# Kernel tuning notes

Hardware: AMD Instinct MI355X
Metric: run time of the kernel (lower is better)

Reference implementation:

```python
import jax, jax.numpy as jnp
import numpy as np

DIM = 1024
INNER = DIM // 2
DSTATE = 8
KSZ = 3
DTRANK = max(INNER // 8, 4)
B, L = 4, 4096


def setup_inputs() -> dict:
    key = jax.random.key(0)
    ks = jax.random.split(key, 8)
    s = 0.02
    x = jax.random.normal(ks[0], (B, L, DIM), dtype=jnp.float32)
    W_in = jax.random.normal(ks[1], (DIM, DIM), dtype=jnp.float32) * s
    Kx = jax.random.normal(ks[2], (INNER, 1, KSZ), dtype=jnp.float32) * 0.1
    Kz = jax.random.normal(ks[3], (INNER, 1, KSZ), dtype=jnp.float32) * 0.1
    W_xproj = jax.random.normal(ks[4], (DTRANK + 2 * DSTATE, INNER), dtype=jnp.float32) * s
    W_dt = jax.random.normal(ks[5], (INNER, DTRANK), dtype=jnp.float32) * s
    # dt bias: inverse_softplus of exp(linspace(log dt_min, log dt_max))
    dt_init = jnp.exp(jnp.linspace(jnp.log(0.02), jnp.log(0.2), INNER))
    b_dt = jnp.log(jnp.expm1(dt_init)).astype(jnp.float32)
    A_log = jnp.log(jnp.tile(jnp.arange(1, DSTATE + 1, dtype=jnp.float32), (INNER, 1)))
    D = jnp.ones((INNER,), dtype=jnp.float32)
    W_out = jax.random.normal(ks[6], (DIM, DIM), dtype=jnp.float32) * s
    return {"x": x, "W_in": W_in, "Kx": Kx, "Kz": Kz, "W_xproj": W_xproj,
            "W_dt": W_dt, "b_dt": b_dt, "A_log": A_log, "D": D, "W_out": W_out}


def _dwconv_silu(u, kern):
    # u: [B,L,C], kern: [C,1,K] depthwise (groups=C), 'same' padding
    c = u.shape[-1]
    v = jnp.transpose(u, (0, 2, 1))  # [B,C,L]
    v = jax.lax.conv_general_dilated(v, kern, (1,), [(KSZ // 2, KSZ // 2)],
                                     dimension_numbers=("NCH", "OIH", "NCH"),
                                     feature_group_count=c)
    return jax.nn.silu(jnp.transpose(v, (0, 2, 1)))


def _forward(x, W_in, Kx, Kz, W_xproj, W_dt, b_dt, A_log, D, W_out):
    h = jnp.einsum("bld,ed->ble", x, W_in)  # Linear(dim,dim), no bias
    xb, zb = jnp.split(h, 2, axis=-1)       # [B,L,INNER] each
    xb = _dwconv_silu(xb, Kx)
    zb = _dwconv_silu(zb, Kz)
    proj = jnp.einsum("blc,oc->blo", xb, W_xproj)
    dt_raw = proj[..., :DTRANK]
    b_raw = proj[..., DTRANK:DTRANK + DSTATE]
    c_raw = proj[..., DTRANK + DSTATE:]
    delta = jnp.clip(jax.nn.softplus(jnp.einsum("blr,cr->blc", dt_raw, W_dt) + b_dt), 1e-4, 1.0)  # [B,L,C]
    b_term = jnp.tanh(b_raw)  # [B,L,N]
    c_term = jnp.tanh(c_raw)  # [B,L,N]
    a = jax.nn.softplus(A_log) + 1e-4  # [C,N]
    decay = jnp.clip(jnp.exp(-delta[..., None] * a), 1e-4, 1.0)        # [B,L,C,N]
    drive = (1.0 - decay) * (b_term[:, :, None, :] * xb[..., None])    # [B,L,C,N]

    def step(state, inp):
        dec_t, drv_t, c_t, x_t = inp  # [B,C,N], [B,C,N], [B,N], [B,C]
        state = dec_t * state + drv_t
        y = jnp.sum(state * c_t[:, None, :], axis=-1) + D * x_t  # [B,C]
        return state, y

    tm = lambda t: jnp.moveaxis(t, 1, 0)  # time-major
    state0 = jnp.zeros((x.shape[0], INNER, DSTATE), dtype=jnp.float32)
    _, ys = jax.lax.scan(step, state0, (tm(decay), tm(drive), tm(c_term), tm(xb)))
    y = jnp.moveaxis(ys, 0, 1)  # [B,L,INNER]
    return jnp.einsum("bld,ed->ble", jnp.concatenate([y, zb], axis=-1), W_out)


def reference(x, W_in, Kx, Kz, W_xproj, W_dt, b_dt, A_log, D, W_out):
    return _forward(x, W_in, Kx, Kz, W_xproj, W_dt, b_dt, A_log, D, W_out)
```

## Files before the change

kernel.cpp:

```cpp
#include <hip/hip_runtime.h>


using bf16x8 = __attribute__((ext_vector_type(8))) short;
using f32x4  = __attribute__((ext_vector_type(4))) float;

__device__ __forceinline__ unsigned short f2bf(float f) {
  unsigned int u = __float_as_uint(f);
  u = u + 0x7fffu + ((u >> 16) & 1u);
  return (unsigned short)(u >> 16);
}

__device__ __forceinline__ float fsoftplus(float x) {
  return (x > 15.f) ? x : __logf(1.f + __expf(x));
}

__device__ __forceinline__ float ftanh(float x) {
  float v = fminf(fmaxf(x, -15.f), 15.f);
  float e = __expf(2.f * v);
  return (e - 1.f) / (e + 1.f);
}

__global__ __launch_bounds__(256) void cvt_bf16_kernel(
    const float* __restrict__ in, unsigned short* __restrict__ out, int n4) {
  int i = blockIdx.x * 256 + threadIdx.x;
  if (i < n4) {
    float4 v = ((const float4*)in)[i];
    ushort4 o;
    o.x = f2bf(v.x); o.y = f2bf(v.y); o.z = f2bf(v.z); o.w = f2bf(v.w);
    ((ushort4*)out)[i] = o;
  }
}

__global__ __launch_bounds__(256) void cvt_wxp_kernel(
    const float* __restrict__ Wx, unsigned short* __restrict__ out) {
  int i = blockIdx.x * 256 + threadIdx.x;
  int row = i >> 9;
  out[i] = (row < 80) ? f2bf(Wx[i]) : (unsigned short)0;
}

__global__ __launch_bounds__(256) void gemm_bt_bf16(
    const unsigned short* __restrict__ A,
    const unsigned short* __restrict__ B,
    float* __restrict__ C, int M, int N, int K) {
  __shared__ short As[128 * 32];
  __shared__ short Bs[128 * 32];
  const int m0 = blockIdx.x * 128;
  const int n0 = blockIdx.y * 128;
  const int lane = threadIdx.x & 63;
  const int wv = threadIdx.x >> 6;
  const int wm = (wv >> 1) * 64;
  const int wn = (wv & 1) * 64;
  f32x4 acc[4][4] = {};
  const int row_a = wv * 32 + (lane >> 2);
  const int koff = (lane & 3) * 8;
  const unsigned short* gA = A + (size_t)(m0 + row_a) * K + koff;
  const unsigned short* gB = B + (size_t)(n0 + row_a) * K + koff;
  short* lA = &As[(wv * 32) * 32];
  short* lB = &Bs[(wv * 32) * 32];
  const int r = lane & 15;
  const int q = lane >> 4;
  for (int k0 = 0; k0 < K; k0 += 32) {
    __syncthreads();
    __builtin_amdgcn_global_load_lds((const __attribute__((address_space(1))) void*)(const void*)gA,
                                     (__attribute__((address_space(3))) void*)(void*)lA, 16, 0, 0);
    __builtin_amdgcn_global_load_lds((const __attribute__((address_space(1))) void*)(const void*)(gA + 16 * K),
                                     (__attribute__((address_space(3))) void*)(void*)(lA + 16 * 32), 16, 0, 0);
    __builtin_amdgcn_global_load_lds((const __attribute__((address_space(1))) void*)(const void*)gB,
                                     (__attribute__((address_space(3))) void*)(void*)lB, 16, 0, 0);
    __builtin_amdgcn_global_load_lds((const __attribute__((address_space(1))) void*)(const void*)(gB + 16 * K),
                                     (__attribute__((address_space(3))) void*)(void*)(lB + 16 * 32), 16, 0, 0);
    gA += 32; gB += 32;
    __syncthreads();
    bf16x8 av[4], bv[4];
#pragma unroll
    for (int i = 0; i < 4; ++i)
      av[i] = *(const bf16x8*)&As[(wm + i * 16 + r) * 32 + q * 8];
#pragma unroll
    for (int j = 0; j < 4; ++j)
      bv[j] = *(const bf16x8*)&Bs[(wn + j * 16 + r) * 32 + q * 8];
#pragma unroll
    for (int i = 0; i < 4; ++i)
#pragma unroll
      for (int j = 0; j < 4; ++j)
        acc[i][j] = __builtin_amdgcn_mfma_f32_16x16x32_bf16(av[i], bv[j], acc[i][j], 0, 0, 0);
  }
#pragma unroll
  for (int i = 0; i < 4; ++i)
#pragma unroll
    for (int j = 0; j < 4; ++j)
#pragma unroll
      for (int t = 0; t < 4; ++t)
        C[(size_t)(m0 + wm + i * 16 + q * 4 + t) * N + (n0 + wn + j * 16 + r)] = acc[i][j][t];
}

__global__ __launch_bounds__(256) void conv_silu_kernel(
    const float* __restrict__ h, const float* __restrict__ Kx, const float* __restrict__ Kz,
    float* __restrict__ xb, unsigned short* __restrict__ xbbf,
    unsigned short* __restrict__ cat) {
  int tid = blockIdx.x * 256 + threadIdx.x;
  int ch = tid & 1023;
  int bl = tid >> 10;
  int l = bl & 4095;
  float k0, k1, k2;
  int c;
  if (ch < 512) { c = ch;       k0 = Kx[c * 3]; k1 = Kx[c * 3 + 1]; k2 = Kx[c * 3 + 2]; }
  else          { c = ch - 512; k0 = Kz[c * 3]; k1 = Kz[c * 3 + 1]; k2 = Kz[c * 3 + 2]; }
  size_t idx = (size_t)bl * 1024 + ch;
  float um = (l > 0)    ? h[idx - 1024] : 0.f;
  float u0 = h[idx];
  float up = (l < 4095) ? h[idx + 1024] : 0.f;
  float v = um * k0 + u0 * k1 + up * k2;
  float o = v / (1.f + __expf(-v));
  if (ch < 512) { xb[(size_t)bl * 512 + c] = o; xbbf[(size_t)bl * 512 + c] = f2bf(o); }
  else          cat[idx] = f2bf(o);
}

__global__ __launch_bounds__(256) void prep_dtbc_kernel(
    const float* __restrict__ proj, unsigned short* __restrict__ dtr,
    float* __restrict__ bterm, float* __restrict__ cterm) {
  int i = blockIdx.x * 256 + threadIdx.x;
  int row = i >> 7, col = i & 127;
  float v = proj[i];
  if (col < 64)      dtr[row * 64 + col] = f2bf(v);
  else if (col < 72) bterm[row * 8 + (col - 64)] = ftanh(v);
  else if (col < 80) cterm[row * 8 + (col - 72)] = ftanh(v);
}

__global__ __launch_bounds__(256) void scan_p1(
    const float* __restrict__ draw, const float* __restrict__ bterm,
    const float* __restrict__ xb, const float* __restrict__ A_log,
    const float* __restrict__ bdt,
    float* __restrict__ Aprod, float* __restrict__ Bpart) {
  int tid = threadIdx.x;
  int gid = blockIdx.x;
  int chunk = gid & 127, half = (gid >> 7) & 1, b = gid >> 8;
  int c = half * 256 + tid;
  float4 a0 = *(const float4*)&A_log[c * 8];
  float4 a1 = *(const float4*)&A_log[c * 8 + 4];
  float na[8] = {a0.x, a0.y, a0.z, a0.w, a1.x, a1.y, a1.z, a1.w};
#pragma unroll
  for (int s = 0; s < 8; ++s) na[s] = -(fsoftplus(na[s]) + 1e-4f);
  float bb = bdt[c];
  int l0 = chunk * 32;
  size_t base  = ((size_t)b * 4096 + l0) * 512 + c;
  size_t bbase = ((size_t)b * 4096 + l0) * 8;
  float S[8] = {}, Ap[8] = {1.f, 1.f, 1.f, 1.f, 1.f, 1.f, 1.f, 1.f};
  for (int i = 0; i < 32; ++i) {
    float dr = draw[base] + bb;
    float xv = xb[base];
    float delta = fminf(fmaxf(fsoftplus(dr), 1e-4f), 1.f);
    float4 bt0 = *(const float4*)&bterm[bbase];
    float4 bt1 = *(const float4*)&bterm[bbase + 4];
    float bt[8] = {bt0.x, bt0.y, bt0.z, bt0.w, bt1.x, bt1.y, bt1.z, bt1.w};
#pragma unroll
    for (int s = 0; s < 8; ++s) {
      float dec = fminf(fmaxf(__expf(delta * na[s]), 1e-4f), 1.f);
      float btx = bt[s] * xv;
      S[s] = dec * S[s] + (btx - dec * btx);
      Ap[s] *= dec;
    }
    base += 512; bbase += 8;
  }
  size_t o = (size_t)chunk * 16384 + ((size_t)(b * 512 + c)) * 8;
  *(float4*)&Aprod[o]     = make_float4(Ap[0], Ap[1], Ap[2], Ap[3]);
  *(float4*)&Aprod[o + 4] = make_float4(Ap[4], Ap[5], Ap[6], Ap[7]);
  *(float4*)&Bpart[o]     = make_float4(S[0], S[1], S[2], S[3]);
  *(float4*)&Bpart[o + 4] = make_float4(S[4], S[5], S[6], S[7]);
}

__global__ __launch_bounds__(256) void scan_p2(
    const float* __restrict__ Aprod, const float* __restrict__ Bpart,
    float* __restrict__ initst) {
  int t = blockIdx.x * 256 + threadIdx.x;
  float st = 0.f;
  for (int ch = 0; ch < 128; ++ch) {
    size_t o = (size_t)ch * 16384 + t;
    initst[o] = st;
    st = Aprod[o] * st + Bpart[o];
  }
}

__global__ __launch_bounds__(256) void scan_p3(
    const float* __restrict__ draw, const float* __restrict__ bterm,
    const float* __restrict__ cterm, const float* __restrict__ xb,
    const float* __restrict__ A_log, const float* __restrict__ bdt,
    const float* __restrict__ Dp,
    const float* __restrict__ initst, unsigned short* __restrict__ cat) {
  int tid = threadIdx.x;
  int gid = blockIdx.x;
  int chunk = gid & 127, half = (gid >> 7) & 1, b = gid >> 8;
  int c = half * 256 + tid;
  float4 a0 = *(const float4*)&A_log[c * 8];
  float4 a1 = *(const float4*)&A_log[c * 8 + 4];
  float na[8] = {a0.x, a0.y, a0.z, a0.w, a1.x, a1.y, a1.z, a1.w};
#pragma unroll
  for (int s = 0; s < 8; ++s) na[s] = -(fsoftplus(na[s]) + 1e-4f);
  float bb = bdt[c];
  float Dv = Dp[c];
  size_t o = (size_t)chunk * 16384 + ((size_t)(b * 512 + c)) * 8;
  float4 s0 = *(const float4*)&initst[o];
  float4 s1 = *(const float4*)&initst[o + 4];
  float S[8] = {s0.x, s0.y, s0.z, s0.w, s1.x, s1.y, s1.z, s1.w};
  int l0 = chunk * 32;
  size_t base  = ((size_t)b * 4096 + l0) * 512 + c;
  size_t bbase = ((size_t)b * 4096 + l0) * 8;
  size_t cbase = ((size_t)b * 4096 + l0) * 1024 + c;
  for (int i = 0; i < 32; ++i) {
    float dr = draw[base] + bb;
    float xv = xb[base];
    float delta = fminf(fmaxf(fsoftplus(dr), 1e-4f), 1.f);
    float4 bt0 = *(const float4*)&bterm[bbase];
    float4 bt1 = *(const float4*)&bterm[bbase + 4];
    float4 ct0 = *(const float4*)&cterm[bbase];
    float4 ct1 = *(const float4*)&cterm[bbase + 4];
    float bt[8] = {bt0.x, bt0.y, bt0.z, bt0.w, bt1.x, bt1.y, bt1.z, bt1.w};
    float ct[8] = {ct0.x, ct0.y, ct0.z, ct0.w, ct1.x, ct1.y, ct1.z, ct1.w};
    float acc = Dv * xv;
#pragma unroll
    for (int s = 0; s < 8; ++s) {
      float dec = fminf(fmaxf(__expf(delta * na[s]), 1e-4f), 1.f);
      float btx = bt[s] * xv;
      S[s] = dec * S[s] + (btx - dec * btx);
      acc += S[s] * ct[s];
    }
    cat[cbase] = f2bf(acc);
    base += 512; bbase += 8; cbase += 1024;
  }
}

extern "C" void kernel_launch(void* const* d_in, const int* in_sizes, int n_in,
                              void* d_out, int out_size, void* d_ws, size_t ws_size,
                              hipStream_t stream) {
  (void)in_sizes; (void)n_in; (void)out_size; (void)ws_size;
  const float* x       = (const float*)d_in[0];
  const float* W_in    = (const float*)d_in[1];
  const float* Kx      = (const float*)d_in[2];
  const float* Kz      = (const float*)d_in[3];
  const float* W_xproj = (const float*)d_in[4];
  const float* W_dt    = (const float*)d_in[5];
  const float* b_dt    = (const float*)d_in[6];
  const float* A_log   = (const float*)d_in[7];
  const float* Dp      = (const float*)d_in[8];
  const float* W_out   = (const float*)d_in[9];
  float* out = (float*)d_out;

  char* w = (char*)d_ws;
  unsigned short* xbf  = (unsigned short*)(w);
  float* xb    = (float*)(w + 33554432);
  float* draw  = (float*)(w + 67108864);
  float* bterm = (float*)(w + 100663296);
  float* cterm = (float*)(w + 101187584);
  float* Aprod = (float*)(w + 101711872);
  float* Bpart = (float*)(w + 110100480);
  float* initst = (float*)(w + 118489088);
  unsigned short* winbf  = (unsigned short*)(w + 126877696);
  unsigned short* woutbf = (unsigned short*)(w + 128974848);
  unsigned short* dtr    = (unsigned short*)(w + 131072000);
  unsigned short* wxp_bf = (unsigned short*)(w + 133169152);
  unsigned short* wd_bf  = (unsigned short*)(w + 133300224);
  unsigned short* xbbf = (unsigned short*)Aprod;
  float* proj = draw;
  float* h = out;

  cvt_bf16_kernel<<<16384, 256, 0, stream>>>(x, xbf, 4194304);
  cvt_bf16_kernel<<<1024, 256, 0, stream>>>(W_in, winbf, 262144);
  cvt_bf16_kernel<<<1024, 256, 0, stream>>>(W_out, woutbf, 262144);
  cvt_bf16_kernel<<<32, 256, 0, stream>>>(W_dt, wd_bf, 8192);
  cvt_wxp_kernel<<<256, 256, 0, stream>>>(W_xproj, wxp_bf);

  gemm_bt_bf16<<<dim3(128, 8), 256, 0, stream>>>(xbf, winbf, h, 16384, 1024, 1024);

  conv_silu_kernel<<<65536, 256, 0, stream>>>(h, Kx, Kz, xb, xbbf, xbf );

  gemm_bt_bf16<<<dim3(128, 1), 256, 0, stream>>>(xbbf, wxp_bf, proj, 16384, 128, 512);
  prep_dtbc_kernel<<<8192, 256, 0, stream>>>(proj, dtr, bterm, cterm);
  gemm_bt_bf16<<<dim3(128, 4), 256, 0, stream>>>(dtr, wd_bf, draw, 16384, 512, 64);

  scan_p1<<<1024, 256, 0, stream>>>(draw, bterm, xb, A_log, b_dt, Aprod, Bpart);
  scan_p2<<<64, 256, 0, stream>>>(Aprod, Bpart, initst);
  scan_p3<<<1024, 256, 0, stream>>>(draw, bterm, cterm, xb, A_log, b_dt, Dp, initst, xbf );

  gemm_bt_bf16<<<dim3(128, 8), 256, 0, stream>>>(xbf, woutbf, out, 16384, 1024, 1024);
}
```

Measured before the change: 370.0 us.

## Replace large GEMMs with 256x256-tile pipelined kernel using direct global-to-LDS loads

Adds a new GEMM kernel with 256x256 output tiles, 512 threads, and an 8-slot LDS ring filled by global_load_lds. It interleaves prefetch of future K tiles with MFMA phases, coordinated by explicit waitcnt, barriers and setprio. Both 1024x1024 projection GEMMs now use it instead of the 128-tile kernel. The goal is more data reuse per block and better overlap of memory traffic with matrix math. In exchange it brings complex hand-tuned synchronisation, higher register pressure and a fixed tile-shape assumption.

```diff
diff --git a/kernel.cpp b/kernel.cpp
--- a/kernel.cpp
+++ b/kernel.cpp
@@ -93,6 +93,116 @@
         C[(size_t)(m0 + wm + i * 16 + q * 4 + t) * N + (n0 + wn + j * 16 + r)] = acc[i][j][t];
 }
 
+__device__ __forceinline__ void g256_stage(short* lds, int slot,
+    const unsigned short* sp, int ktIdx, int wvLds) {
+  const unsigned short* s = sp + ktIdx * 64;
+  __builtin_amdgcn_global_load_lds((const __attribute__((address_space(1))) void*)s,
+      (__attribute__((address_space(3))) void*)(lds + slot * 8192 + wvLds), 16, 0, 0);
+  __builtin_amdgcn_global_load_lds((const __attribute__((address_space(1))) void*)(s + 32),
+      (__attribute__((address_space(3))) void*)(lds + slot * 8192 + 4096 + wvLds), 16, 0, 0);
+}
+
+template <int PAR, int MH, int NHLO, bool RA, bool RB, int SSLOT, bool VM, bool HINT>
+__device__ __forceinline__ void g256_phase(
+    short* lds, int aSlotOff, int bSlotOff, int aoff, int boff, int wvLds,
+    bf16x8 (&av)[4][2], bf16x8 (&bv)[4][2], f32x4 (&acc)[8][4],
+    const unsigned short* sp, int ktIdx) {
+  if (RA) {
+#pragma unroll
+    for (int ii = 0; ii < 4; ++ii)
+#pragma unroll
+      for (int ks = 0; ks < 2; ++ks)
+        av[ii][ks] = *(const bf16x8*)&lds[PAR * 4 * 8192 + aSlotOff + ks * 4096 +
+                                          (MH * 4 + ii) * 512 + aoff];
+  }
+  if (RB) {
+#pragma unroll
+    for (int jj = 0; jj < 2; ++jj)
+#pragma unroll
+      for (int ks = 0; ks < 2; ++ks)
+        bv[NHLO + jj][ks] = *(const bf16x8*)&lds[(PAR * 4 + 2) * 8192 + bSlotOff + ks * 4096 +
+                                                 (NHLO + jj) * 512 + boff];
+  }
+  g256_stage(lds, SSLOT, sp, ktIdx, wvLds);
+  if (HINT) asm volatile("s_waitcnt lgkmcnt(8)");
+  if (VM) asm volatile("s_waitcnt vmcnt(4)" ::: "memory");
+  __builtin_amdgcn_s_barrier();
+  asm volatile("s_waitcnt lgkmcnt(0)" ::: "memory");
+  __builtin_amdgcn_s_setprio(1);
+#pragma unroll
+  for (int ii = 0; ii < 4; ++ii)
+#pragma unroll
+    for (int jj = 0; jj < 2; ++jj) {
+      acc[MH * 4 + ii][NHLO + jj] = __builtin_amdgcn_mfma_f32_16x16x32_bf16(
+          av[ii][0], bv[NHLO + jj][0], acc[MH * 4 + ii][NHLO + jj], 0, 0, 0);
+      acc[MH * 4 + ii][NHLO + jj] = __builtin_amdgcn_mfma_f32_16x16x32_bf16(
+          av[ii][1], bv[NHLO + jj][1], acc[MH * 4 + ii][NHLO + jj], 0, 0, 0);
+    }
+  __builtin_amdgcn_s_setprio(0);
+  __builtin_amdgcn_s_barrier();
+}
+
+__global__ __launch_bounds__(512, 2) void gemm256_bt(
+    const unsigned short* __restrict__ A,
+    const unsigned short* __restrict__ B,
+    float* __restrict__ C, int M, int N, int K) {
+  __shared__ short lds[8 * 8192];
+  const int nmt = M >> 8;
+  const int bid = blockIdx.x;
+  const int swz = (bid & 7) * ((int)gridDim.x >> 3) + (bid >> 3);
+  const int mtile = swz % nmt, ntile = swz / nmt;
+  const int m0 = mtile << 8, n0 = ntile << 8;
+  const int tid = threadIdx.x;
+  const int w = tid >> 6, lane = tid & 63;
+  const int r = lane & 15, q = lane >> 4;
+  const int wrow = w >> 2, wcol = w & 3;
+  const int trow = tid >> 2, tcol = (tid & 3) << 3;
+  const unsigned short* pA0 = A + (size_t)(m0 + trow) * K + tcol;
+  const unsigned short* pA1 = pA0 + (size_t)128 * K;
+  const unsigned short* pB0 = B + (size_t)(n0 + trow) * K + tcol;
+  const unsigned short* pB1 = pB0 + (size_t)128 * K;
+  const int wvLds = w * 512;
+  const int aSlotOff = wrow * 8192;
+  const int bSlotOff = (wcol >> 1) * 8192;
+  const int aoff = r * 32 + q * 8;
+  const int boff = (wcol & 1) * 2048 + r * 32 + q * 8;
+  bf16x8 av[4][2], bv[4][2];
+  f32x4 acc[8][4] = {};
+  const int NT = K >> 6;
+  const int NI = NT >> 1;
+  g256_stage(lds, 0, pA0, 0, wvLds);
+  g256_stage(lds, 1, pA1, 0, wvLds);
+  g256_stage(lds, 2, pB0, 0, wvLds);
+  g256_stage(lds, 3, pB1, 0, wvLds);
+  g256_stage(lds, 6, pB0, 1, wvLds);
+  g256_stage(lds, 7, pB1, 1, wvLds);
+  asm volatile("s_waitcnt vmcnt(4)" ::: "memory");
+  __builtin_amdgcn_s_barrier();
+#pragma unroll 1
+  for (int it = 0; it < NI; ++it) {
+    const int ktO  = 2 * it + 1;
+    const int ktE2 = (2 * it + 2 < NT) ? 2 * it + 2 : NT - 1;
+    const int ktO2 = (2 * it + 3 < NT) ? 2 * it + 3 : NT - 1;
+    g256_phase<0, 0, 0, true,  true,  4, false, true >(lds, aSlotOff, bSlotOff, aoff, boff, wvLds, av, bv, acc, pA0, ktO);
+    g256_phase<0, 0, 2, false, true,  5, false, false>(lds, aSlotOff, bSlotOff, aoff, boff, wvLds, av, bv, acc, pA1, ktO);
+    g256_phase<0, 1, 2, true,  false, 2, false, false>(lds, aSlotOff, bSlotOff, aoff, boff, wvLds, av, bv, acc, pB0, ktE2);
+    g256_phase<0, 1, 0, false, false, 0, true,  false>(lds, aSlotOff, bSlotOff, aoff, boff, wvLds, av, bv, acc, pA0, ktE2);
+    g256_phase<1, 0, 0, true,  true,  1, false, true >(lds, aSlotOff, bSlotOff, aoff, boff, wvLds, av, bv, acc, pA1, ktE2);
+    g256_phase<1, 0, 2, false, true,  3, false, false>(lds, aSlotOff, bSlotOff, aoff, boff, wvLds, av, bv, acc, pB1, ktE2);
+    g256_phase<1, 1, 2, true,  false, 6, false, false>(lds, aSlotOff, bSlotOff, aoff, boff, wvLds, av, bv, acc, pB0, ktO2);
+    g256_phase<1, 1, 0, false, false, 7, true,  false>(lds, aSlotOff, bSlotOff, aoff, boff, wvLds, av, bv, acc, pB1, ktO2);
+  }
+  asm volatile("s_waitcnt vmcnt(0) lgkmcnt(0)" ::: "memory");
+  float* Cw = C + (size_t)(m0 + wrow * 128) * N + n0 + wcol * 64;
+#pragma unroll
+  for (int ii = 0; ii < 8; ++ii)
+#pragma unroll
+    for (int jj = 0; jj < 4; ++jj)
+#pragma unroll
+      for (int t = 0; t < 4; ++t)
+        Cw[(size_t)(ii * 16 + q * 4 + t) * N + jj * 16 + r] = acc[ii][jj][t];
+}
+
 __global__ __launch_bounds__(256) void conv_silu_kernel(
     const float* __restrict__ h, const float* __restrict__ Kx, const float* __restrict__ Kz,
     float* __restrict__ xb, unsigned short* __restrict__ xbbf,
@@ -268,7 +378,7 @@
   cvt_bf16_kernel<<<32, 256, 0, stream>>>(W_dt, wd_bf, 8192);
   cvt_wxp_kernel<<<256, 256, 0, stream>>>(W_xproj, wxp_bf);
 
-  gemm_bt_bf16<<<dim3(128, 8), 256, 0, stream>>>(xbf, winbf, h, 16384, 1024, 1024);
+  gemm256_bt<<<256, 512, 0, stream>>>(xbf, winbf, h, 16384, 1024, 1024);
 
   conv_silu_kernel<<<65536, 256, 0, stream>>>(h, Kx, Kz, xb, xbbf, xbf );
 
@@ -280,5 +390,5 @@
   scan_p2<<<64, 256, 0, stream>>>(Aprod, Bpart, initst);
   scan_p3<<<1024, 256, 0, stream>>>(draw, bterm, cterm, xb, A_log, b_dt, Dp, initst, xbf );
 
-  gemm_bt_bf16<<<dim3(128, 8), 256, 0, stream>>>(xbf, woutbf, out, 16384, 1024, 1024);
-}
+  gemm256_bt<<<256, 512, 0, stream>>>(xbf, woutbf, out, 16384, 1024, 1024);
+}
```

Result: faster. 351.6 us (-5.0%).
